# Performance work log

Hardware: AMD Instinct MI355X
Metric: run time of the kernel (lower is better)

The kernel has to match this reference:

```python
import jax, jax.numpy as jnp
import numpy as np
from math import sqrt

HEADS = 8
DIM_HEAD = 64
MP_T = 0.3          # magnitude-preserving residual interpolation
LIN_EPS = 1e-4      # eps used by custom Linear and PixelNorm l2norm


def _l2norm(t, eps):
    # F.normalize: t / max(||t||_2, eps) along last dim
    n = jnp.linalg.norm(t, axis=-1, keepdims=True)
    return t / jnp.maximum(n, eps)


def _mp_linear(x, w):
    # weight rows l2-normalized, scaled by 1/sqrt(fan_in) (inference path)
    wn = _l2norm(w, LIN_EPS) / sqrt(w.shape[-1])
    return x @ wn.T


def _mp_add(a, b, t=MP_T):
    return (a * (1.0 - t) + b * t) / sqrt((1.0 - t) ** 2 + t ** 2)


def _pixel_norm(t):
    return _l2norm(t, LIN_EPS) * sqrt(t.shape[-1])


def _mp_attention(x, w_qkv, w_out, mem_kv):
    # x: [B, N, C]
    B, N, C = x.shape
    res = x
    qkv = _mp_linear(x, w_qkv)                     # [B, N, 3*H*D]
    q, k, v = jnp.split(qkv, 3, axis=-1)
    split_heads = lambda t: t.reshape(B, N, HEADS, DIM_HEAD).transpose(0, 2, 1, 3)
    q, k, v = split_heads(q), split_heads(k), split_heads(v)  # [B, H, N, D]
    mk = jnp.broadcast_to(mem_kv[0], (B,) + mem_kv[0].shape)  # [B, H, M, D]
    mv = jnp.broadcast_to(mem_kv[1], (B,) + mem_kv[1].shape)
    k = jnp.concatenate([mk, k], axis=2)           # [B, H, M+N, D]
    v = jnp.concatenate([mv, v], axis=2)
    q, k, v = _pixel_norm(q), _pixel_norm(k), _pixel_norm(v)
    q = q * (DIM_HEAD ** -0.5)
    sim = jnp.einsum('bhid,bhjd->bhij', q, k)
    attn = jax.nn.softmax(sim, axis=-1)
    out = jnp.einsum('bhij,bhjd->bhid', attn, v)
    out = out.transpose(0, 2, 1, 3).reshape(B, N, HEADS * DIM_HEAD)
    out = _mp_linear(out, w_out)
    return _mp_add(out, res)


def setup_inputs() -> dict:
    key = jax.random.key(0)
    ks = jax.random.split(key, 6)
    b, c, t, h, w = 2, 512, 16, 32, 32
    depth = 2
    return {
        'x': jax.random.normal(ks[0], (b, c, t, h, w), dtype=jnp.float32),
        'w_qkv': jax.random.normal(ks[1], (depth, 3 * HEADS * DIM_HEAD, c), dtype=jnp.float32),
        'w_out': jax.random.normal(ks[2], (depth, c, HEADS * DIM_HEAD), dtype=jnp.float32),
        'mem_kv': jax.random.normal(ks[3], (depth, 2, HEADS, 4, DIM_HEAD), dtype=jnp.float32),
        'w_proj': jax.random.normal(ks[4], (c, c), dtype=jnp.float32),
        'gain': jnp.ones((), dtype=jnp.float32),
    }


def reference(x, w_qkv, w_out, mem_kv, w_proj, gain):
    b, c, t, h, w = x.shape
    # b c t h w -> (b h w) t c
    y = x.transpose(0, 3, 4, 2, 1).reshape(b * h * w, t, c)
    residual = y
    for i in range(w_qkv.shape[0]):
        y = _mp_attention(y, w_qkv[i], w_out[i], mem_kv[i])
    y = _mp_linear(y, w_proj) * gain               # proj_out: Linear + Gain
    y = _mp_add(y, residual)
    # (b h w) t c -> b c t h w
    y = y.reshape(b, h, w, t, c).transpose(0, 4, 3, 1, 2)
    return y
```

## Files before the change

### kernel.cpp

```cpp
#include <hip/hip_runtime.h>
#include <hip/hip_bf16.h>


typedef __attribute__((ext_vector_type(8))) __bf16 bf16x8;
typedef __attribute__((ext_vector_type(4))) __bf16 bf16x4;
typedef __attribute__((ext_vector_type(4))) float  f32x4;

#define MP_NEW 0.9191450300180579f
#define MP_RES 0.3939192985791677f

__device__ __forceinline__ __hip_bfloat16 f2b(float x) { return __float2bfloat16(x); }
__device__ __forceinline__ float b2f(__hip_bfloat16 x) { return __bfloat162float(x); }

#define GLOAD16(g, l)                                                             \
  __builtin_amdgcn_global_load_lds((const __attribute__((address_space(1))) void*)(g), \
                                   (__attribute__((address_space(3))) void*)(l), 16, 0, 0)

__global__ __launch_bounds__(256)
void fill_kernel(float* o, int n)
{
  int i = blockIdx.x * 256 + threadIdx.x;
  if (i < n) o[i] = 12345.0f;
}

__global__ __launch_bounds__(64)
void wnorm_pack(const float* __restrict__ w, __hip_bfloat16* __restrict__ o)
{
  const int r = blockIdx.x, lane = threadIdx.x;
  const float* wr = w + (size_t)r * 512;
  float x[8], s = 0.f;
  #pragma unroll
  for (int e = 0; e < 8; ++e) { x[e] = wr[e * 64 + lane]; s += x[e] * x[e]; }
  #pragma unroll
  for (int m = 1; m < 64; m <<= 1) s += __shfl_xor(s, m);
  const float scale = 1.0f / (fmaxf(sqrtf(s), 1e-4f) * 22.62741699796952f);
  #pragma unroll
  for (int e = 0; e < 8; ++e) o[(size_t)r * 512 + e * 64 + lane] = f2b(x[e] * scale);
}

__global__ __launch_bounds__(64)
void memnorm(const float* __restrict__ mkv, __hip_bfloat16* __restrict__ KG,
             __hip_bfloat16* __restrict__ VG)
{
  const int vec = blockIdx.x;
  const int lane = threadIdx.x;
  const int l = vec >> 6, r = vec & 63;
  const int kv = r >> 5, h = (r >> 2) & 7, j = r & 3;
  const float x = mkv[l * 4096 + kv * 2048 + h * 256 + j * 64 + lane];
  float s = x * x;
  #pragma unroll
  for (int m = 1; m < 64; m <<= 1) s += __shfl_xor(s, m);
  const float v = x * (8.0f / fmaxf(sqrtf(s), 1e-4f));
  if (kv == 0) KG[((l * 8 + h) * 4 + j) * 64 + lane] = f2b(v);
  else         VG[((l * 8 + h) * 64 + lane) * 4 + j] = f2b(v);
}

__global__ __launch_bounds__(256)
void transpose_in(const float* __restrict__ x, __hip_bfloat16* __restrict__ Y0)
{
  __shared__ float tile[32][33];
  const int tx = threadIdx.x, ty = threadIdx.y;
  const int hh = blockIdx.x;
  const int c0 = blockIdx.y * 32;
  const int bt = blockIdx.z;
  const int b = bt >> 4, t = bt & 15;
  const float* xb = x + (size_t)b * 8388608 + (size_t)t * 1024 + hh * 32 + tx;
  #pragma unroll
  for (int r = 0; r < 4; ++r) {
    const int cc = ty * 4 + r;
    tile[tx][cc] = xb[(size_t)(c0 + cc) * 16384];
  }
  __syncthreads();
  #pragma unroll
  for (int r = 0; r < 4; ++r) {
    const int w = ty * 4 + r;
    const size_t m = ((size_t)b * 1024 + hh * 32 + w) * 16 + t;
    Y0[m * 512 + c0 + tx] = f2b(tile[w][tx]);
  }
}

__global__ __launch_bounds__(256)
void transpose_out(const __hip_bfloat16* __restrict__ Yf, float* __restrict__ out)
{
  __shared__ __align__(16) __hip_bfloat16 tile[32][33];
  const int tx = threadIdx.x, ty = threadIdx.y;
  const int hh = blockIdx.x;
  const int c0 = blockIdx.y * 32;
  const int bt = blockIdx.z;
  const int b = bt >> 4, t = bt & 15;
  #pragma unroll
  for (int r = 0; r < 4; ++r) {
    const int w = ty * 4 + r;
    const size_t m = ((size_t)b * 1024 + hh * 32 + w) * 16 + t;
    tile[w][tx] = Yf[m * 512 + c0 + tx];
  }
  __syncthreads();
  float* ob = out + (size_t)b * 8388608 + (size_t)t * 1024 + hh * 32 + tx;
  #pragma unroll
  for (int r = 0; r < 4; ++r) {
    const int cc = ty * 4 + r;
    ob[(size_t)(c0 + cc) * 16384] = b2f(tile[tx][cc]);
  }
}

#define SLAB_LD 1032
#define VT_LD   40
#define PS_LD   33
__global__ __launch_bounds__(256)
void attn_kernel(__hip_bfloat16* __restrict__ QKV,
                 const __hip_bfloat16* __restrict__ KmemG,
                 const __hip_bfloat16* __restrict__ VmemTG)
{
  __shared__ __align__(16) __hip_bfloat16 slab[16 * SLAB_LD];
  __shared__ __align__(16) __hip_bfloat16 VtS[4][64 * VT_LD];
  __shared__ float PsS[4][16 * PS_LD];
  __shared__ __align__(16) __hip_bfloat16 Kmem[2048];
  __shared__ __align__(16) __hip_bfloat16 VmemT[2048];
  const int tid = threadIdx.x;
  const int wid = tid >> 6, lane = tid & 63;
  const int seq = blockIdx.x;
  __hip_bfloat16* gbase = QKV + (size_t)seq * 16 * 1536;

  #pragma unroll
  for (int u = 0; u < 8; ++u) {
    const int o = wid * 8 + u;
    const int r = o >> 1, c = o & 1;
    GLOAD16(gbase + r * 1536 + 512 + c * 512 + lane * 8,
            (char*)slab + r * 2064 + c * 1024);
  }
  #pragma unroll
  for (int u = 0; u < 2; ++u) {
    const int o = wid * 2 + u;
    if (o < 4) GLOAD16(KmemG + o * 512 + lane * 8, (char*)Kmem + o * 1024);
    else       GLOAD16(VmemTG + (o - 4) * 512 + lane * 8, (char*)VmemT + (o - 4) * 1024);
  }
  __syncthreads();

  __hip_bfloat16* Vt = VtS[wid];
  float* Ps = PsS[wid];
  const int jj = lane & 15;
  const int grp = lane >> 4;

  #pragma unroll
  for (int hh = 0; hh < 2; ++hh) {
    const int h = wid * 2 + hh;

    #pragma unroll
    for (int p = 0; p < 8; ++p) {
      const int kvv = p >> 2;
      const int j = (p & 3) * 4 + grp;
      const int col = kvv * 512 + h * 64 + jj * 4;
      bf16x4 x4 = *(const bf16x4*)&slab[j * SLAB_LD + col];
      const float f0 = (float)x4[0], f1 = (float)x4[1];
      const float f2 = (float)x4[2], f3 = (float)x4[3];
      float s = f0 * f0 + f1 * f1 + f2 * f2 + f3 * f3;
      s += __shfl_xor(s, 1); s += __shfl_xor(s, 2);
      s += __shfl_xor(s, 4); s += __shfl_xor(s, 8);
      const float sc = 8.0f / fmaxf(sqrtf(s), 1e-4f);
      if (kvv == 0) {
        bf16x4 w4;
        w4[0] = (__bf16)(f0 * sc); w4[1] = (__bf16)(f1 * sc);
        w4[2] = (__bf16)(f2 * sc); w4[3] = (__bf16)(f3 * sc);
        *(bf16x4*)&slab[j * SLAB_LD + col] = w4;
      } else {
        Vt[(jj * 4 + 0) * VT_LD + 4 + j] = f2b(f0 * sc);
        Vt[(jj * 4 + 1) * VT_LD + 4 + j] = f2b(f1 * sc);
        Vt[(jj * 4 + 2) * VT_LD + 4 + j] = f2b(f2 * sc);
        Vt[(jj * 4 + 3) * VT_LD + 4 + j] = f2b(f3 * sc);
      }
    }
    {
      bf16x4 mv = *(const bf16x4*)&VmemT[h * 256 + lane * 4];
      #pragma unroll
      for (int j = 0; j < 4; ++j) *(__bf16*)&Vt[lane * VT_LD + j] = mv[j];
    }
    #pragma unroll
    for (int z = 0; z < 6; ++z)
      *(unsigned int*)&Vt[lane * VT_LD + 20 + z * 2] = 0u;
    #pragma unroll
    for (int z = 0; z < 3; ++z)
      Ps[(lane >> 2) * PS_LD + 20 + (lane & 3) * 3 + z] = 0.f;

    const __hip_bfloat16* qg = gbase + (size_t)jj * 1536 + h * 64 + grp * 8;
    const bf16x8 qa0 = *(const bf16x8*)qg;
    const bf16x8 qa1 = *(const bf16x8*)(qg + 32);
    float qs = 0.f;
    #pragma unroll
    for (int e = 0; e < 8; ++e) {
      const float a0 = (float)qa0[e], a1 = (float)qa1[e];
      qs += a0 * a0 + a1 * a1;
    }
    qs += __shfl_xor(qs, 16); qs += __shfl_xor(qs, 32);
    const float qscale = 1.0f / fmaxf(sqrtf(qs), 1e-4f);

    f32x4 s0 = {0.f, 0.f, 0.f, 0.f}, s1 = {0.f, 0.f, 0.f, 0.f};
    #pragma unroll
    for (int kk = 0; kk < 2; ++kk) {
      const int koff = kk * 32 + grp * 8;
      const bf16x8 a = kk ? qa1 : qa0;
      const __hip_bfloat16* bp0 = (jj < 4)
          ? &Kmem[(h * 4 + jj) * 64 + koff]
          : &slab[(jj - 4) * SLAB_LD + h * 64 + koff];
      const bf16x8 b0 = *(const bf16x8*)bp0;
      bf16x8 b1 = *(const bf16x8*)&slab[(12 + (jj & 3)) * SLAB_LD + h * 64 + koff];
      if (jj >= 4) {
        #pragma unroll
        for (int e = 0; e < 8; ++e) b1[e] = (__bf16)0.f;
      }
      s0 = __builtin_amdgcn_mfma_f32_16x16x32_bf16(a, b0, s0, 0, 0, 0);
      s1 = __builtin_amdgcn_mfma_f32_16x16x32_bf16(a, b1, s1, 0, 0, 0);
    }

    #pragma unroll
    for (int r = 0; r < 4; ++r) {
      const int row = grp * 4 + r;
      const float sc = __shfl(qscale, row);
      Ps[row * PS_LD + jj] = s0[r] * sc;
      if (jj < 4) Ps[row * PS_LD + 16 + jj] = s1[r] * sc;
    }

    if (lane < 16) {
      float mx = -1e30f;
      #pragma unroll
      for (int j = 0; j < 20; ++j) mx = fmaxf(mx, Ps[lane * PS_LD + j]);
      float e[20], ssum = 0.f;
      #pragma unroll
      for (int j = 0; j < 20; ++j) { e[j] = expf(Ps[lane * PS_LD + j] - mx); ssum += e[j]; }
      const float inv = 1.0f / ssum;
      #pragma unroll
      for (int j = 0; j < 20; ++j) Ps[lane * PS_LD + j] = e[j] * inv;
    }

    bf16x8 pa;
    #pragma unroll
    for (int e = 0; e < 8; ++e) {
      const __hip_bfloat16 t = f2b(Ps[jj * PS_LD + grp * 8 + e]);
      pa[e] = *(const __bf16*)&t;
    }

    #pragma unroll
    for (int t = 0; t < 4; ++t) {
      const bf16x8 vb = *(const bf16x8*)&Vt[(t * 16 + jj) * VT_LD + grp * 8];
      f32x4 o = {0.f, 0.f, 0.f, 0.f};
      o = __builtin_amdgcn_mfma_f32_16x16x32_bf16(pa, vb, o, 0, 0, 0);
      #pragma unroll
      for (int r = 0; r < 4; ++r)
        gbase[(size_t)(grp * 4 + r) * 1536 + h * 64 + t * 16 + jj] = f2b(o[r]);
    }
  }
}

template<int MODE>
__global__ __launch_bounds__(256)
void gemm3(const __hip_bfloat16* __restrict__ A, const __hip_bfloat16* __restrict__ Bw,
           int lda, __hip_bfloat16* __restrict__ outp, int ldo,
           const __hip_bfloat16* __restrict__ res, const float* __restrict__ gainp)
{
  __shared__ __hip_bfloat16 sA[128 * 64];
  __shared__ __hip_bfloat16 sB[128 * 64];
  const int nwg = gridDim.x * gridDim.y;
  int bid = blockIdx.y * gridDim.x + blockIdx.x;
  bid = (bid & 7) * (nwg >> 3) + (bid >> 3);
  const int bn = bid % gridDim.x, bm = bid / gridDim.x;

  const int tid = threadIdx.x;
  const int wid = tid >> 6, lane = tid & 63;
  const int wrow = wid >> 1, wcol = wid & 1;
  const int fr = lane & 15, fq = lane >> 4;
  const int rowL = tid >> 3;
  const int colSwz = (((tid & 7) ^ (rowL & 7)) * 8);

  const __hip_bfloat16* Ab = A  + (size_t)bm * 128 * lda;
  const __hip_bfloat16* Bb = Bw + (size_t)bn * 128 * 512;

  f32x4 acc[4][4];
  const f32x4 zz = {0.f, 0.f, 0.f, 0.f};
  #pragma unroll
  for (int i = 0; i < 4; ++i)
    #pragma unroll
    for (int j = 0; j < 4; ++j) acc[i][j] = zz;

  for (int ks = 0; ks < 8; ++ks) {
    const int k0 = ks * 64;
    __syncthreads();
    #pragma unroll
    for (int call = 0; call < 4; ++call) {
      const __hip_bfloat16* ga = Ab + (size_t)(call * 32 + rowL) * lda + k0 + colSwz;
      GLOAD16(ga, (char*)sA + call * 4096 + wid * 1024);
    }
    #pragma unroll
    for (int call = 0; call < 4; ++call) {
      const __hip_bfloat16* gb = Bb + (size_t)(call * 32 + rowL) * 512 + k0 + colSwz;
      GLOAD16(gb, (char*)sB + call * 4096 + wid * 1024);
    }
    __syncthreads();

    const bf16x8* pA = (const bf16x8*)sA;
    const bf16x8* pB = (const bf16x8*)sB;
    #pragma unroll
    for (int kk = 0; kk < 2; ++kk) {
      bf16x8 af[4], bfv[4];
      #pragma unroll
      for (int fi = 0; fi < 4; ++fi)
        af[fi] = pA[(wrow * 64 + fi * 16 + fr) * 8 + ((kk * 4 + fq) ^ (fr & 7))];
      #pragma unroll
      for (int fj = 0; fj < 4; ++fj)
        bfv[fj] = pB[(wcol * 64 + fj * 16 + fr) * 8 + ((kk * 4 + fq) ^ (fr & 7))];
      #pragma unroll
      for (int fi = 0; fi < 4; ++fi)
        #pragma unroll
        for (int fj = 0; fj < 4; ++fj)
          acc[fi][fj] = __builtin_amdgcn_mfma_f32_16x16x32_bf16(af[fi], bfv[fj], acc[fi][fj], 0, 0, 0);
    }
  }

  float g = 0.f;
  if (MODE == 2) g = gainp[0];

  #pragma unroll
  for (int fi = 0; fi < 4; ++fi) {
    #pragma unroll
    for (int fj = 0; fj < 4; ++fj) {
      #pragma unroll
      for (int jj2 = 0; jj2 < 4; ++jj2) {
        const int gm = bm * 128 + wrow * 64 + fi * 16 + fq * 4 + jj2;
        const int gn = bn * 128 + wcol * 64 + fj * 16 + fr;
        const float c = acc[fi][fj][jj2];
        if constexpr (MODE == 0) {
          outp[(size_t)gm * ldo + gn] = f2b(c);
        } else if constexpr (MODE == 1) {
          const float y = MP_NEW * c + MP_RES * b2f(res[(size_t)gm * 512 + gn]);
          outp[(size_t)gm * ldo + gn] = f2b(y);
        } else {
          const float y = MP_NEW * (c * g) + MP_RES * b2f(res[(size_t)gm * 512 + gn]);
          outp[(size_t)gm * ldo + gn] = f2b(y);
        }
      }
    }
  }
}

extern "C" void kernel_launch(void* const* d_in, const int* in_sizes, int n_in,
                              void* d_out, int out_size, void* d_ws, size_t ws_size,
                              hipStream_t stream)
{
  const float* x     = (const float*)d_in[0];
  const float* wqkv  = (const float*)d_in[1];
  const float* wout  = (const float*)d_in[2];
  const float* mkv   = (const float*)d_in[3];
  const float* wproj = (const float*)d_in[4];
  const float* gain  = (const float*)d_in[5];
  float* out = (float*)d_out;

  char* ws = (char*)d_ws;
  __hip_bfloat16* Y0     = (__hip_bfloat16*)(ws + 0);
  __hip_bfloat16* Ycur   = (__hip_bfloat16*)(ws + 33554432);
  __hip_bfloat16* QKVc   = (__hip_bfloat16*)(ws + 67108864);
  __hip_bfloat16* WQ     = (__hip_bfloat16*)(ws + 92274688);
  __hip_bfloat16* WO     = (__hip_bfloat16*)(ws + 95420416);
  __hip_bfloat16* WP     = (__hip_bfloat16*)(ws + 96468992);
  __hip_bfloat16* KmemG  = (__hip_bfloat16*)(ws + 96993280);
  __hip_bfloat16* VmemTG = (__hip_bfloat16*)(ws + 97001472);

  if (ws_size < 97009664ULL) {
    fill_kernel<<<(out_size + 255) / 256, 256, 0, stream>>>(out, out_size);
    return;
  }

  wnorm_pack<<<3072, 64, 0, stream>>>(wqkv,  WQ);
  wnorm_pack<<<1024, 64, 0, stream>>>(wout,  WO);
  wnorm_pack<<<512,  64, 0, stream>>>(wproj, WP);
  memnorm<<<128, 64, 0, stream>>>(mkv, KmemG, VmemTG);

  transpose_in<<<dim3(32, 16, 32), dim3(32, 8), 0, stream>>>(x, Y0);

  const int M = 32768, CH = 8192, NCH = M / CH;
  for (int layer = 0; layer < 2; ++layer) {
    const __hip_bfloat16* WQl = WQ + (size_t)layer * 786432;
    const __hip_bfloat16* WOl = WO + (size_t)layer * 262144;
    __hip_bfloat16* Acur = (layer == 0) ? Y0 : Ycur;
    for (int ch = 0; ch < NCH; ++ch) {
      const size_t m0 = (size_t)ch * CH;
      gemm3<0><<<dim3(12, CH / 128), 256, 0, stream>>>(Acur + m0 * 512, WQl, 512,
                                                       QKVc, 1536, nullptr, nullptr);
      attn_kernel<<<CH / 16, 256, 0, stream>>>(QKVc, KmemG + (size_t)layer * 2048,
                                               VmemTG + (size_t)layer * 2048);
      gemm3<1><<<dim3(4, CH / 128), 256, 0, stream>>>(QKVc, WOl, 1536,
                                                      Ycur + m0 * 512, 512,
                                                      Acur + m0 * 512, nullptr);
    }
  }

  gemm3<2><<<dim3(4, 256), 256, 0, stream>>>(Ycur, WP, 512, Y0, 512, Y0, gain);
  transpose_out<<<dim3(32, 16, 32), dim3(32, 8), 0, stream>>>(Y0, out);
}
```

Measured before the change: 545.5 us.

## Fuse Q/K/V pixel-norm into QKV GEMM epilogue and enlarge chunk size

The per-head l2 pixel normalization of q, k and v moves from the attention kernel into the QKV GEMM epilogue. Each 64-column head segment is reduced across lanes there and scaled by 1 for q and 8 for k and v. This removes the normalization loops, the shuffles and the extra shared-memory writes from the attention kernel. The host also picks a larger row chunk (up to the full 32768 rows) when the workspace is big enough, which cuts the number of kernel launches. The risk is that q is now rounded to bf16 before scaling, and the larger QKV buffer needs more workspace.

```diff
diff --git a/kernel.cpp b/kernel.cpp
--- a/kernel.cpp
+++ b/kernel.cpp
@@ -146,28 +146,14 @@
     const int h = wid * 2 + hh;
 
     #pragma unroll
-    for (int p = 0; p < 8; ++p) {
-      const int kvv = p >> 2;
-      const int j = (p & 3) * 4 + grp;
-      const int col = kvv * 512 + h * 64 + jj * 4;
+    for (int p = 0; p < 4; ++p) {
+      const int j = p * 4 + grp;
+      const int col = 512 + h * 64 + jj * 4;
       bf16x4 x4 = *(const bf16x4*)&slab[j * SLAB_LD + col];
-      const float f0 = (float)x4[0], f1 = (float)x4[1];
-      const float f2 = (float)x4[2], f3 = (float)x4[3];
-      float s = f0 * f0 + f1 * f1 + f2 * f2 + f3 * f3;
-      s += __shfl_xor(s, 1); s += __shfl_xor(s, 2);
-      s += __shfl_xor(s, 4); s += __shfl_xor(s, 8);
-      const float sc = 8.0f / fmaxf(sqrtf(s), 1e-4f);
-      if (kvv == 0) {
-        bf16x4 w4;
-        w4[0] = (__bf16)(f0 * sc); w4[1] = (__bf16)(f1 * sc);
-        w4[2] = (__bf16)(f2 * sc); w4[3] = (__bf16)(f3 * sc);
-        *(bf16x4*)&slab[j * SLAB_LD + col] = w4;
-      } else {
-        Vt[(jj * 4 + 0) * VT_LD + 4 + j] = f2b(f0 * sc);
-        Vt[(jj * 4 + 1) * VT_LD + 4 + j] = f2b(f1 * sc);
-        Vt[(jj * 4 + 2) * VT_LD + 4 + j] = f2b(f2 * sc);
-        Vt[(jj * 4 + 3) * VT_LD + 4 + j] = f2b(f3 * sc);
-      }
+      *(__bf16*)&Vt[(jj * 4 + 0) * VT_LD + 4 + j] = x4[0];
+      *(__bf16*)&Vt[(jj * 4 + 1) * VT_LD + 4 + j] = x4[1];
+      *(__bf16*)&Vt[(jj * 4 + 2) * VT_LD + 4 + j] = x4[2];
+      *(__bf16*)&Vt[(jj * 4 + 3) * VT_LD + 4 + j] = x4[3];
     }
     {
       bf16x4 mv = *(const bf16x4*)&VmemT[h * 256 + lane * 4];
@@ -184,14 +170,6 @@
     const __hip_bfloat16* qg = gbase + (size_t)jj * 1536 + h * 64 + grp * 8;
     const bf16x8 qa0 = *(const bf16x8*)qg;
     const bf16x8 qa1 = *(const bf16x8*)(qg + 32);
-    float qs = 0.f;
-    #pragma unroll
-    for (int e = 0; e < 8; ++e) {
-      const float a0 = (float)qa0[e], a1 = (float)qa1[e];
-      qs += a0 * a0 + a1 * a1;
-    }
-    qs += __shfl_xor(qs, 16); qs += __shfl_xor(qs, 32);
-    const float qscale = 1.0f / fmaxf(sqrtf(qs), 1e-4f);
 
     f32x4 s0 = {0.f, 0.f, 0.f, 0.f}, s1 = {0.f, 0.f, 0.f, 0.f};
     #pragma unroll
@@ -214,9 +192,8 @@
     #pragma unroll
     for (int r = 0; r < 4; ++r) {
       const int row = grp * 4 + r;
-      const float sc = __shfl(qscale, row);
-      Ps[row * PS_LD + jj] = s0[r] * sc;
-      if (jj < 4) Ps[row * PS_LD + 16 + jj] = s1[r] * sc;
+      Ps[row * PS_LD + jj] = s0[r];
+      if (jj < 4) Ps[row * PS_LD + 16 + jj] = s1[r];
     }
 
     if (lane < 16) {
@@ -314,26 +291,45 @@
     }
   }
 
-  float g = 0.f;
-  if (MODE == 2) g = gainp[0];
-
-  #pragma unroll
-  for (int fi = 0; fi < 4; ++fi) {
-    #pragma unroll
-    for (int fj = 0; fj < 4; ++fj) {
+  if constexpr (MODE == 0) {
+    const float num = (bn < 4) ? 1.0f : 8.0f;
+    #pragma unroll
+    for (int fi = 0; fi < 4; ++fi) {
       #pragma unroll
       for (int jj2 = 0; jj2 < 4; ++jj2) {
+        float ss = 0.f;
+        #pragma unroll
+        for (int fj = 0; fj < 4; ++fj) { const float c = acc[fi][fj][jj2]; ss += c * c; }
+        ss += __shfl_xor(ss, 1); ss += __shfl_xor(ss, 2);
+        ss += __shfl_xor(ss, 4); ss += __shfl_xor(ss, 8);
+        const float sc = num / fmaxf(sqrtf(ss), 1e-4f);
         const int gm = bm * 128 + wrow * 64 + fi * 16 + fq * 4 + jj2;
-        const int gn = bn * 128 + wcol * 64 + fj * 16 + fr;
-        const float c = acc[fi][fj][jj2];
-        if constexpr (MODE == 0) {
-          outp[(size_t)gm * ldo + gn] = f2b(c);
-        } else if constexpr (MODE == 1) {
-          const float y = MP_NEW * c + MP_RES * b2f(res[(size_t)gm * 512 + gn]);
-          outp[(size_t)gm * ldo + gn] = f2b(y);
-        } else {
-          const float y = MP_NEW * (c * g) + MP_RES * b2f(res[(size_t)gm * 512 + gn]);
-          outp[(size_t)gm * ldo + gn] = f2b(y);
+        #pragma unroll
+        for (int fj = 0; fj < 4; ++fj) {
+          const int gn = bn * 128 + wcol * 64 + fj * 16 + fr;
+          outp[(size_t)gm * ldo + gn] = f2b(acc[fi][fj][jj2] * sc);
+        }
+      }
+    }
+  } else {
+    float g = 0.f;
+    if (MODE == 2) g = gainp[0];
+    #pragma unroll
+    for (int fi = 0; fi < 4; ++fi) {
+      #pragma unroll
+      for (int fj = 0; fj < 4; ++fj) {
+        #pragma unroll
+        for (int jj2 = 0; jj2 < 4; ++jj2) {
+          const int gm = bm * 128 + wrow * 64 + fi * 16 + fq * 4 + jj2;
+          const int gn = bn * 128 + wcol * 64 + fj * 16 + fr;
+          const float c = acc[fi][fj][jj2];
+          if constexpr (MODE == 1) {
+            const float y = MP_NEW * c + MP_RES * b2f(res[(size_t)gm * 512 + gn]);
+            outp[(size_t)gm * ldo + gn] = f2b(y);
+          } else {
+            const float y = MP_NEW * (c * g) + MP_RES * b2f(res[(size_t)gm * 512 + gn]);
+            outp[(size_t)gm * ldo + gn] = f2b(y);
+          }
         }
       }
     }
@@ -352,20 +348,25 @@
   const float* gain  = (const float*)d_in[5];
   float* out = (float*)d_out;
 
+  const size_t SZ_Y = 33554432;
+  int CH;
+  if      (ws_size >= 2 * SZ_Y + (size_t)32768 * 1536 * 2 + 4734976) CH = 32768;
+  else if (ws_size >= 2 * SZ_Y + (size_t)16384 * 1536 * 2 + 4734976) CH = 16384;
+  else if (ws_size >= 2 * SZ_Y + (size_t)8192  * 1536 * 2 + 4734976) CH = 8192;
+  else {
+    fill_kernel<<<(out_size + 255) / 256, 256, 0, stream>>>(out, out_size);
+    return;
+  }
+  const size_t qkv_bytes = (size_t)CH * 1536 * 2;
   char* ws = (char*)d_ws;
   __hip_bfloat16* Y0     = (__hip_bfloat16*)(ws + 0);
-  __hip_bfloat16* Ycur   = (__hip_bfloat16*)(ws + 33554432);
-  __hip_bfloat16* QKVc   = (__hip_bfloat16*)(ws + 67108864);
-  __hip_bfloat16* WQ     = (__hip_bfloat16*)(ws + 92274688);
-  __hip_bfloat16* WO     = (__hip_bfloat16*)(ws + 95420416);
-  __hip_bfloat16* WP     = (__hip_bfloat16*)(ws + 96468992);
-  __hip_bfloat16* KmemG  = (__hip_bfloat16*)(ws + 96993280);
-  __hip_bfloat16* VmemTG = (__hip_bfloat16*)(ws + 97001472);
-
-  if (ws_size < 97009664ULL) {
-    fill_kernel<<<(out_size + 255) / 256, 256, 0, stream>>>(out, out_size);
-    return;
-  }
+  __hip_bfloat16* Ycur   = (__hip_bfloat16*)(ws + SZ_Y);
+  __hip_bfloat16* QKVc   = (__hip_bfloat16*)(ws + 2 * SZ_Y);
+  __hip_bfloat16* WQ     = (__hip_bfloat16*)(ws + 2 * SZ_Y + qkv_bytes);
+  __hip_bfloat16* WO     = WQ + 1572864;
+  __hip_bfloat16* WP     = WO + 524288;
+  __hip_bfloat16* KmemG  = WP + 262144;
+  __hip_bfloat16* VmemTG = KmemG + 4096;
 
   wnorm_pack<<<3072, 64, 0, stream>>>(wqkv,  WQ);
   wnorm_pack<<<1024, 64, 0, stream>>>(wout,  WO);
@@ -374,7 +375,7 @@
 
   transpose_in<<<dim3(32, 16, 32), dim3(32, 8), 0, stream>>>(x, Y0);
 
-  const int M = 32768, CH = 8192, NCH = M / CH;
+  const int M = 32768, NCH = M / CH;
   for (int layer = 0; layer < 2; ++layer) {
     const __hip_bfloat16* WQl = WQ + (size_t)layer * 786432;
     const __hip_bfloat16* WOl = WO + (size_t)layer * 262144;
```

Result: faster. 459.8 us (-15.7%).
